# Optimization experiments

Hardware: AMD Instinct MI355X
Metric: run time of the kernel (lower is better)

Reference implementation:

```python
import jax, jax.numpy as jnp
import numpy as np

EMB_SIZE = 768
BLOCK_SIZE = 64
NUM_CLASS = 97
N = 4096
NUM_BLOCKS = EMB_SIZE // BLOCK_SIZE  # 12


def setup_inputs() -> dict:
    key = jax.random.key(0)
    k1, k2, k3 = jax.random.split(key, 3)
    head_embeddings = jax.random.normal(k1, (N, EMB_SIZE), dtype=jnp.float32)
    tail_embeddings = jax.random.normal(k2, (N, EMB_SIZE), dtype=jnp.float32)
    # xavier_uniform for [NUM_CLASS, EMB_SIZE*BLOCK_SIZE]
    fan_in = EMB_SIZE * BLOCK_SIZE
    fan_out = NUM_CLASS
    bound = float(np.sqrt(6.0 / (fan_in + fan_out)))
    W = jax.random.uniform(k3, (NUM_CLASS, EMB_SIZE * BLOCK_SIZE), dtype=jnp.float32,
                           minval=-bound, maxval=bound)
    b = jnp.full((NUM_CLASS,), 0.1, dtype=jnp.float32)
    return {"head_embeddings": head_embeddings, "tail_embeddings": tail_embeddings,
            "W": W, "b": b}


def reference(head_embeddings, tail_embeddings, W, b):
    n = head_embeddings.shape[0]
    b1 = head_embeddings.reshape(n, NUM_BLOCKS, BLOCK_SIZE)  # [N, K, S]
    b2 = tail_embeddings.reshape(n, NUM_BLOCKS, BLOCK_SIZE)  # [N, K, S]
    # block-wise outer product: [N, K, S, S] -> [N, K*S*S]
    bl = jnp.einsum('nki,nkj->nkij', b1, b2).reshape(n, EMB_SIZE * BLOCK_SIZE)
    logits = bl @ W.T + b  # [N, NUM_CLASS]
    return logits
```

## Files before the change

### kernel.cpp

```cpp
#include <hip/hip_runtime.h>
#include <hip/hip_bf16.h>
#include <stdint.h>

#define NROWS 4096
#define NCLS  97
#define EMB   768
#define KTOT  49152
#define OUT_ELEMS (NROWS * NCLS)
#define E_ELEMS  (NROWS * EMB)
#define NK32  (KTOT / 32)
#define WT_BYTES ((size_t)NK32 * 128 * 64)

typedef __attribute__((ext_vector_type(8)))  short short8;
typedef __attribute__((ext_vector_type(4)))  float floatx4;
typedef __bf16 bf16x2 __attribute__((ext_vector_type(2)));
typedef __bf16 bf16x8 __attribute__((ext_vector_type(8)));

__device__ __forceinline__ uint4 cvt8(float4 a, float4 b) {
  bf16x8 v;
  v[0] = (__bf16)a.x; v[1] = (__bf16)a.y; v[2] = (__bf16)a.z; v[3] = (__bf16)a.w;
  v[4] = (__bf16)b.x; v[5] = (__bf16)b.y; v[6] = (__bf16)b.z; v[7] = (__bf16)b.w;
  return __builtin_bit_cast(uint4, v);
}

__device__ __forceinline__ uint32_t mkbf2(float lo, float hi) {
  bf16x2 v; v[0] = (__bf16)lo; v[1] = (__bf16)hi;
  return __builtin_bit_cast(uint32_t, v);
}

__global__ void prep(const float* __restrict__ W, uint4* __restrict__ wt)
{
  const int nwt = NK32 * 128 * 4;
  int t = blockIdx.x * blockDim.x + threadIdx.x;
  if (t >= nwt) return;
  int eo = t & 3;
  int c  = (t >> 2) & 127;
  int kc = t >> 9;
  uint4 v = uint4{0u, 0u, 0u, 0u};
  if (c < NCLS) {
    const float4* p = (const float4*)(W + (size_t)c * KTOT + kc * 32 + eo * 8);
    v = cvt8(p[0], p[1]);
  }
  wt[t] = v;
}

__global__ __launch_bounds__(256, 2)
void bilinear_main(const float* __restrict__ b1f,
                   const float* __restrict__ b2f,
                   const char* __restrict__ Wt,
                   const float* __restrict__ biasg,
                   float* __restrict__ P,
                   float* __restrict__ outd,
                   int klen)
{
  const int tid  = threadIdx.x;
  const int w    = tid >> 6;
  const int l    = tid & 63;
  const int l15  = l & 15;
  const int quad = l >> 4;
  const int mhalf = w & 1;
  const int chalf = w >> 1;
  const bool cfull = (chalf == 0);
  const int bm = blockIdx.y;
  const int k0 = blockIdx.x * klen;

  int nrow[4];
#pragma unroll
  for (int rt = 0; rt < 4; ++rt) nrow[rt] = bm * 128 + mhalf * 64 + rt * 16 + l15;

  const char* wtl = Wt + (size_t)(k0 >> 5) * 8192
                       + (chalf * 64 + l15) * 64 + quad * 16;

  floatx4 acc[4][4];
#pragma unroll
  for (int rt = 0; rt < 4; ++rt)
#pragma unroll
    for (int ct = 0; ct < 4; ++ct)
      acc[rt][ct] = floatx4{0.f, 0.f, 0.f, 0.f};

  float b2r[4][2][8];
  int cur_k = -1;
  const int nwin = klen >> 6;

  for (int gwin = 0; gwin < nwin; gwin += 8) {
    const int kap0 = k0 + (gwin << 6);
    const int kblk = kap0 >> 12;
    const int i0   = (kap0 >> 6) & 63;
    if (kblk != cur_k) {
      cur_k = kblk;
#pragma unroll
      for (int rt = 0; rt < 4; ++rt)
#pragma unroll
        for (int kh = 0; kh < 2; ++kh) {
          const float* p = b2f + (size_t)nrow[rt] * EMB + kblk * 64 + kh * 32 + quad * 8;
          float4 v0 = ((const float4*)p)[0];
          float4 v1 = ((const float4*)p)[1];
          b2r[rt][kh][0] = v0.x; b2r[rt][kh][1] = v0.y;
          b2r[rt][kh][2] = v0.z; b2r[rt][kh][3] = v0.w;
          b2r[rt][kh][4] = v1.x; b2r[rt][kh][5] = v1.y;
          b2r[rt][kh][6] = v1.z; b2r[rt][kh][7] = v1.w;
        }
    }

#pragma unroll
    for (int ih = 0; ih < 2; ++ih) {
      float4 b1v[4];
#pragma unroll
      for (int rt = 0; rt < 4; ++rt)
        b1v[rt] = *(const float4*)(b1f + (size_t)nrow[rt] * EMB +
                                   kblk * 64 + i0 + ih * 4);

#pragma unroll
      for (int ii2 = 0; ii2 < 4; ++ii2) {
        const int iw = gwin + ih * 4 + ii2;
        const char* pw = wtl + (size_t)iw * 16384;

        float s[4];
#pragma unroll
        for (int rt = 0; rt < 4; ++rt)
          s[rt] = (&b1v[rt].x)[ii2];

#pragma unroll
        for (int kh = 0; kh < 2; ++kh) {
          short8 wf[4];
#pragma unroll
          for (int ct = 0; ct < 4; ++ct)
            if (ct < 3 || cfull)
              wf[ct] = __builtin_bit_cast(short8,
                         *(const uint4*)(pw + kh * 8192 + ct * 1024));
#pragma unroll
          for (int rt = 0; rt < 4; ++rt) {
            uint4 afr;
            afr.x = mkbf2(b2r[rt][kh][0] * s[rt], b2r[rt][kh][1] * s[rt]);
            afr.y = mkbf2(b2r[rt][kh][2] * s[rt], b2r[rt][kh][3] * s[rt]);
            afr.z = mkbf2(b2r[rt][kh][4] * s[rt], b2r[rt][kh][5] * s[rt]);
            afr.w = mkbf2(b2r[rt][kh][6] * s[rt], b2r[rt][kh][7] * s[rt]);
            short8 af = __builtin_bit_cast(short8, afr);
#pragma unroll
            for (int ct = 0; ct < 4; ++ct)
              if (ct < 3 || cfull)
                acc[rt][ct] = __builtin_amdgcn_mfma_f32_16x16x32_bf16(
                                  af, wf[ct], acc[rt][ct], 0, 0, 0);
          }
        }
      }
    }
  }

  if (P) {
    float* Pb = P + (size_t)blockIdx.x * OUT_ELEMS;
#pragma unroll
    for (int rt = 0; rt < 4; ++rt)
#pragma unroll
      for (int ct = 0; ct < 4; ++ct) {
        const int c = chalf * 64 + ct * 16 + l15;
        if (c < NCLS) {
#pragma unroll
          for (int r = 0; r < 4; ++r) {
            const int row = bm * 128 + mhalf * 64 + rt * 16 + quad * 4 + r;
            Pb[(size_t)row * NCLS + c] = acc[rt][ct][r];
          }
        }
      }
  } else {
#pragma unroll
    for (int rt = 0; rt < 4; ++rt)
#pragma unroll
      for (int ct = 0; ct < 4; ++ct) {
        const int c = chalf * 64 + ct * 16 + l15;
        if (c < NCLS) {
          const float bv = biasg[c];
#pragma unroll
          for (int r = 0; r < 4; ++r) {
            const int row = bm * 128 + mhalf * 64 + rt * 16 + quad * 4 + r;
            outd[(size_t)row * NCLS + c] = acc[rt][ct][r] + bv;
          }
        }
      }
  }
}

template<int KSC>
__global__ void reduce_bias_t(const float* __restrict__ P,
                              const float* __restrict__ biasg,
                              float* __restrict__ out)
{
  int i = blockIdx.x * blockDim.x + threadIdx.x;
  const int n4 = OUT_ELEMS / 4;
  if (i >= n4) return;
  int c0 = (i * 4) % NCLS;
  int c1 = c0 + 1 == NCLS ? 0 : c0 + 1;
  int c2 = c1 + 1 == NCLS ? 0 : c1 + 1;
  int c3 = c2 + 1 == NCLS ? 0 : c2 + 1;
  float4 s;
  s.x = biasg[c0]; s.y = biasg[c1]; s.z = biasg[c2]; s.w = biasg[c3];
  const float4* P4 = (const float4*)P;
#pragma unroll
  for (int t = 0; t < KSC; ++t) {
    float4 v = P4[(size_t)t * n4 + i];
    s.x += v.x; s.y += v.y; s.z += v.z; s.w += v.w;
  }
  ((float4*)out)[i] = s;
}

static void launch_reduce(int KS, const float* P, const float* bb, float* out,
                          hipStream_t stream) {
  const int nb = (OUT_ELEMS / 4 + 255) / 256;
  switch (KS) {
    case 16: reduce_bias_t<16><<<nb, 256, 0, stream>>>(P, bb, out); break;
    case 12: reduce_bias_t<12><<<nb, 256, 0, stream>>>(P, bb, out); break;
    case 8:  reduce_bias_t<8><<<nb, 256, 0, stream>>>(P, bb, out);  break;
    case 6:  reduce_bias_t<6><<<nb, 256, 0, stream>>>(P, bb, out);  break;
    case 4:  reduce_bias_t<4><<<nb, 256, 0, stream>>>(P, bb, out);  break;
    case 3:  reduce_bias_t<3><<<nb, 256, 0, stream>>>(P, bb, out);  break;
    case 2:  reduce_bias_t<2><<<nb, 256, 0, stream>>>(P, bb, out);  break;
    default: reduce_bias_t<1><<<nb, 256, 0, stream>>>(P, bb, out);  break;
  }
}

extern "C" void kernel_launch(void* const* d_in, const int* in_sizes, int n_in,
                              void* d_out, int out_size, void* d_ws, size_t ws_size,
                              hipStream_t stream) {
  const float* b1f = (const float*)d_in[0];
  const float* b2f = (const float*)d_in[1];
  const float* Wf  = (const float*)d_in[2];
  const float* bbf = (const float*)d_in[3];
  float* out = (float*)d_out;

  const size_t slice = (size_t)OUT_ELEMS * 4;
  static const int cands[] = {16, 12, 8, 6, 4, 3, 2, 1};
  const int NC = 8;

  int KS = 0;
  for (int i = 0; i < NC; ++i)
    if (WT_BYTES + (size_t)cands[i] * slice <= ws_size) { KS = cands[i]; break; }

  uint4* Wt = (uint4*)d_ws;
  const int nwt = NK32 * 128 * 4;

  prep<<<(nwt + 255) / 256, 256, 0, stream>>>(Wf, Wt);

  if (KS > 0) {
    float* P = (float*)((char*)d_ws + WT_BYTES);
    bilinear_main<<<dim3(KS, 32), 256, 0, stream>>>(
        b1f, b2f, (const char*)Wt, bbf, P, nullptr, KTOT / KS);
    launch_reduce(KS, P, bbf, out, stream);
  } else {
    bilinear_main<<<dim3(1, 32), 256, 0, stream>>>(
        b1f, b2f, (const char*)Wt, bbf, nullptr, out, KTOT);
  }
}
```

Measured before the change: 152.8 us.

## Switch to fp16 MFMA with packed fp16 A-build and double-buffered W fragment loads

Replaces the bf16 path with fp16: W is pre-converted to fp16, b2 is held as packed fp16 pairs, and the A fragment is built with packed half multiplies instead of fp32 multiplies plus bf16 conversion. This cuts the VALU work per MFMA. It also adds register double-buffering, loading the next window's W fragments before computing the current one so global-load latency overlaps MFMA work. The cost is more register pressure and fp16 range and precision risk: products are formed in fp16, where values can overflow or lose accuracy.

Result: no change. 151.9 us (-0.6%).

```diff
diff --git a/kernel.cpp b/kernel.cpp
--- a/kernel.cpp
+++ b/kernel.cpp
@@ -11,21 +11,15 @@
 #define NK32  (KTOT / 32)
 #define WT_BYTES ((size_t)NK32 * 128 * 64)
 
-typedef __attribute__((ext_vector_type(8)))  short short8;
 typedef __attribute__((ext_vector_type(4)))  float floatx4;
-typedef __bf16 bf16x2 __attribute__((ext_vector_type(2)));
-typedef __bf16 bf16x8 __attribute__((ext_vector_type(8)));
-
-__device__ __forceinline__ uint4 cvt8(float4 a, float4 b) {
-  bf16x8 v;
-  v[0] = (__bf16)a.x; v[1] = (__bf16)a.y; v[2] = (__bf16)a.z; v[3] = (__bf16)a.w;
-  v[4] = (__bf16)b.x; v[5] = (__bf16)b.y; v[6] = (__bf16)b.z; v[7] = (__bf16)b.w;
+typedef _Float16 f16x2 __attribute__((ext_vector_type(2)));
+typedef _Float16 f16x8 __attribute__((ext_vector_type(8)));
+
+__device__ __forceinline__ uint4 cvt8h(float4 a, float4 b) {
+  f16x8 v;
+  v[0] = (_Float16)a.x; v[1] = (_Float16)a.y; v[2] = (_Float16)a.z; v[3] = (_Float16)a.w;
+  v[4] = (_Float16)b.x; v[5] = (_Float16)b.y; v[6] = (_Float16)b.z; v[7] = (_Float16)b.w;
   return __builtin_bit_cast(uint4, v);
-}
-
-__device__ __forceinline__ uint32_t mkbf2(float lo, float hi) {
-  bf16x2 v; v[0] = (__bf16)lo; v[1] = (__bf16)hi;
-  return __builtin_bit_cast(uint32_t, v);
 }
 
 __global__ void prep(const float* __restrict__ W, uint4* __restrict__ wt)
@@ -39,7 +33,7 @@
   uint4 v = uint4{0u, 0u, 0u, 0u};
   if (c < NCLS) {
     const float4* p = (const float4*)(W + (size_t)c * KTOT + kc * 32 + eo * 8);
-    v = cvt8(p[0], p[1]);
+    v = cvt8h(p[0], p[1]);
   }
   wt[t] = v;
 }
@@ -78,9 +72,49 @@
     for (int ct = 0; ct < 4; ++ct)
       acc[rt][ct] = floatx4{0.f, 0.f, 0.f, 0.f};
 
-  float b2r[4][2][8];
+  f16x2 b2h[4][2][4];
+  f16x2 sv[4];
+  uint4 wfA[2][4], wfB[2][4];
+
+#define LOADWF(buf, iwv)  do {                                              \
+    const char* pw_ = wtl + (size_t)(iwv) * 16384;                          \
+    _Pragma("unroll")                                                       \
+    for (int kh_ = 0; kh_ < 2; ++kh_)                                       \
+      _Pragma("unroll")                                                     \
+      for (int ct_ = 0; ct_ < 4; ++ct_)                                     \
+        if (ct_ < 3 || cfull)                                               \
+          buf[kh_][ct_] = *(const uint4*)(pw_ + kh_ * 8192 + ct_ * 1024);   \
+  } while (0)
+
+#define COMPUTE(buf)  do {                                                  \
+    _Pragma("unroll")                                                       \
+    for (int kh_ = 0; kh_ < 2; ++kh_) {                                     \
+      _Pragma("unroll")                                                     \
+      for (int rt_ = 0; rt_ < 4; ++rt_) {                                   \
+        f16x2 p0 = sv[rt_] * b2h[rt_][kh_][0];                              \
+        f16x2 p1 = sv[rt_] * b2h[rt_][kh_][1];                              \
+        f16x2 p2 = sv[rt_] * b2h[rt_][kh_][2];                              \
+        f16x2 p3 = sv[rt_] * b2h[rt_][kh_][3];                              \
+        uint4 au;                                                           \
+        au.x = __builtin_bit_cast(uint32_t, p0);                            \
+        au.y = __builtin_bit_cast(uint32_t, p1);                            \
+        au.z = __builtin_bit_cast(uint32_t, p2);                            \
+        au.w = __builtin_bit_cast(uint32_t, p3);                            \
+        f16x8 af = __builtin_bit_cast(f16x8, au);                           \
+        _Pragma("unroll")                                                   \
+        for (int ct_ = 0; ct_ < 4; ++ct_)                                   \
+          if (ct_ < 3 || cfull)                                             \
+            acc[rt_][ct_] = __builtin_amdgcn_mfma_f32_16x16x32_f16(         \
+                af, __builtin_bit_cast(f16x8, buf[kh_][ct_]),               \
+                acc[rt_][ct_], 0, 0, 0);                                    \
+      }                                                                     \
+    }                                                                       \
+  } while (0)
+
   int cur_k = -1;
   const int nwin = klen >> 6;
+
+  LOADWF(wfA, 0);
 
   for (int gwin = 0; gwin < nwin; gwin += 8) {
     const int kap0 = k0 + (gwin << 6);
@@ -95,10 +129,10 @@
           const float* p = b2f + (size_t)nrow[rt] * EMB + kblk * 64 + kh * 32 + quad * 8;
           float4 v0 = ((const float4*)p)[0];
           float4 v1 = ((const float4*)p)[1];
-          b2r[rt][kh][0] = v0.x; b2r[rt][kh][1] = v0.y;
-          b2r[rt][kh][2] = v0.z; b2r[rt][kh][3] = v0.w;
-          b2r[rt][kh][4] = v1.x; b2r[rt][kh][5] = v1.y;
-          b2r[rt][kh][6] = v1.z; b2r[rt][kh][7] = v1.w;
+          b2h[rt][kh][0][0] = (_Float16)v0.x; b2h[rt][kh][0][1] = (_Float16)v0.y;
+          b2h[rt][kh][1][0] = (_Float16)v0.z; b2h[rt][kh][1][1] = (_Float16)v0.w;
+          b2h[rt][kh][2][0] = (_Float16)v1.x; b2h[rt][kh][2][1] = (_Float16)v1.y;
+          b2h[rt][kh][3][0] = (_Float16)v1.z; b2h[rt][kh][3][1] = (_Float16)v1.w;
         }
     }
 
@@ -112,40 +146,24 @@
 
 #pragma unroll
       for (int ii2 = 0; ii2 < 4; ++ii2) {
-        const int iw = gwin + ih * 4 + ii2;
-        const char* pw = wtl + (size_t)iw * 16384;
-
-        float s[4];
-#pragma unroll
-        for (int rt = 0; rt < 4; ++rt)
-          s[rt] = (&b1v[rt].x)[ii2];
-
-#pragma unroll
-        for (int kh = 0; kh < 2; ++kh) {
-          short8 wf[4];
-#pragma unroll
-          for (int ct = 0; ct < 4; ++ct)
-            if (ct < 3 || cfull)
-              wf[ct] = __builtin_bit_cast(short8,
-                         *(const uint4*)(pw + kh * 8192 + ct * 1024));
-#pragma unroll
-          for (int rt = 0; rt < 4; ++rt) {
-            uint4 afr;
-            afr.x = mkbf2(b2r[rt][kh][0] * s[rt], b2r[rt][kh][1] * s[rt]);
-            afr.y = mkbf2(b2r[rt][kh][2] * s[rt], b2r[rt][kh][3] * s[rt]);
-            afr.z = mkbf2(b2r[rt][kh][4] * s[rt], b2r[rt][kh][5] * s[rt]);
-            afr.w = mkbf2(b2r[rt][kh][6] * s[rt], b2r[rt][kh][7] * s[rt]);
-            short8 af = __builtin_bit_cast(short8, afr);
-#pragma unroll
-            for (int ct = 0; ct < 4; ++ct)
-              if (ct < 3 || cfull)
-                acc[rt][ct] = __builtin_amdgcn_mfma_f32_16x16x32_bf16(
-                                  af, wf[ct], acc[rt][ct], 0, 0, 0);
-          }
-        }
+        const int s  = ih * 4 + ii2;
+        const int iw = gwin + s;
+        int ipf = iw + 1;
+        if (ipf > nwin - 1) ipf = nwin - 1;
+
+#pragma unroll
+        for (int rt = 0; rt < 4; ++rt) {
+          _Float16 h = (_Float16)((&b1v[rt].x)[ii2]);
+          sv[rt][0] = h; sv[rt][1] = h;
+        }
+
+        if ((s & 1) == 0) { LOADWF(wfB, ipf); COMPUTE(wfA); }
+        else              { LOADWF(wfA, ipf); COMPUTE(wfB); }
       }
     }
   }
+#undef LOADWF
+#undef COMPUTE
 
   if (P) {
     float* Pb = P + (size_t)blockIdx.x * OUT_ELEMS;
```

## Stage W tiles through LDS with register prefetch and switch to fp16 packed math

Applied to the files above, without the earlier changes.

Each block now loads the per-window W tile cooperatively into shared memory, prefetching the next tile into registers while computing the current one. Previously each wave read W fragments straight from global memory. The A-operand outer product now uses packed fp16 multiplies instead of fp32 multiplies plus bf16 conversion, and the MFMA switches to the f16 variant. The change adds two block barriers per window and LDS traffic, and fp16 has a smaller dynamic range than bf16, which could affect accuracy.

Measured after the change: 214.2 us. 1.4x slower.

```diff
diff --git a/kernel.cpp b/kernel.cpp
--- a/kernel.cpp
+++ b/kernel.cpp
@@ -11,21 +11,15 @@
 #define NK32  (KTOT / 32)
 #define WT_BYTES ((size_t)NK32 * 128 * 64)
 
-typedef __attribute__((ext_vector_type(8)))  short short8;
 typedef __attribute__((ext_vector_type(4)))  float floatx4;
-typedef __bf16 bf16x2 __attribute__((ext_vector_type(2)));
-typedef __bf16 bf16x8 __attribute__((ext_vector_type(8)));
-
-__device__ __forceinline__ uint4 cvt8(float4 a, float4 b) {
-  bf16x8 v;
-  v[0] = (__bf16)a.x; v[1] = (__bf16)a.y; v[2] = (__bf16)a.z; v[3] = (__bf16)a.w;
-  v[4] = (__bf16)b.x; v[5] = (__bf16)b.y; v[6] = (__bf16)b.z; v[7] = (__bf16)b.w;
+typedef _Float16 f16x2 __attribute__((ext_vector_type(2)));
+typedef _Float16 f16x8 __attribute__((ext_vector_type(8)));
+
+__device__ __forceinline__ uint4 cvt8h(float4 a, float4 b) {
+  f16x8 v;
+  v[0] = (_Float16)a.x; v[1] = (_Float16)a.y; v[2] = (_Float16)a.z; v[3] = (_Float16)a.w;
+  v[4] = (_Float16)b.x; v[5] = (_Float16)b.y; v[6] = (_Float16)b.z; v[7] = (_Float16)b.w;
   return __builtin_bit_cast(uint4, v);
-}
-
-__device__ __forceinline__ uint32_t mkbf2(float lo, float hi) {
-  bf16x2 v; v[0] = (__bf16)lo; v[1] = (__bf16)hi;
-  return __builtin_bit_cast(uint32_t, v);
 }
 
 __global__ void prep(const float* __restrict__ W, uint4* __restrict__ wt)
@@ -39,7 +33,7 @@
   uint4 v = uint4{0u, 0u, 0u, 0u};
   if (c < NCLS) {
     const float4* p = (const float4*)(W + (size_t)c * KTOT + kc * 32 + eo * 8);
-    v = cvt8(p[0], p[1]);
+    v = cvt8h(p[0], p[1]);
   }
   wt[t] = v;
 }
@@ -64,12 +58,14 @@
   const int bm = blockIdx.y;
   const int k0 = blockIdx.x * klen;
 
+  __shared__ uint4 sW[1024];
+
   int nrow[4];
 #pragma unroll
   for (int rt = 0; rt < 4; ++rt) nrow[rt] = bm * 128 + mhalf * 64 + rt * 16 + l15;
 
-  const char* wtl = Wt + (size_t)(k0 >> 5) * 8192
-                       + (chalf * 64 + l15) * 64 + quad * 16;
+  const char* wtbase = Wt + (size_t)(k0 >> 5) * 8192;
+  const int rslot = chalf * 256 + l15 * 4 + quad;
 
   floatx4 acc[4][4];
 #pragma unroll
@@ -78,74 +74,117 @@
     for (int ct = 0; ct < 4; ++ct)
       acc[rt][ct] = floatx4{0.f, 0.f, 0.f, 0.f};
 
-  float b2r[4][2][8];
-  int cur_k = -1;
+  f16x2 b2h[4][2][4];
+  float4 b1cur[4], b1nxt[4];
+  uint4  wst[4];
+
+#define LOADB2(kbv) do {                                                      \
+    _Pragma("unroll")                                                         \
+    for (int rt_ = 0; rt_ < 4; ++rt_)                                         \
+      _Pragma("unroll")                                                       \
+      for (int kh_ = 0; kh_ < 2; ++kh_) {                                     \
+        const float* p_ = b2f + (size_t)nrow[rt_] * EMB + (kbv) * 64 +        \
+                          kh_ * 32 + quad * 8;                                \
+        float4 v0_ = ((const float4*)p_)[0];                                  \
+        float4 v1_ = ((const float4*)p_)[1];                                  \
+        b2h[rt_][kh_][0][0] = (_Float16)v0_.x; b2h[rt_][kh_][0][1] = (_Float16)v0_.y; \
+        b2h[rt_][kh_][1][0] = (_Float16)v0_.z; b2h[rt_][kh_][1][1] = (_Float16)v0_.w; \
+        b2h[rt_][kh_][2][0] = (_Float16)v1_.x; b2h[rt_][kh_][2][1] = (_Float16)v1_.y; \
+        b2h[rt_][kh_][3][0] = (_Float16)v1_.z; b2h[rt_][kh_][3][1] = (_Float16)v1_.w; \
+      }                                                                       \
+  } while (0)
+
   const int nwin = klen >> 6;
-
-  for (int gwin = 0; gwin < nwin; gwin += 8) {
-    const int kap0 = k0 + (gwin << 6);
-    const int kblk = kap0 >> 12;
-    const int i0   = (kap0 >> 6) & 63;
-    if (kblk != cur_k) {
-      cur_k = kblk;
+  const int ngrp = nwin >> 2;
+
+  {
+    const uint4* g0 = (const uint4*)wtbase;
+#pragma unroll
+    for (int it = 0; it < 4; ++it) wst[it] = g0[it * 256 + tid];
+#pragma unroll
+    for (int it = 0; it < 4; ++it) sW[it * 256 + tid] = wst[it];
+  }
+  int cur_kb = k0 >> 12;
+  LOADB2(cur_kb);
+#pragma unroll
+  for (int rt = 0; rt < 4; ++rt)
+    b1cur[rt] = *(const float4*)(b1f + (size_t)nrow[rt] * EMB +
+                                 cur_kb * 64 + ((k0 >> 6) & 63));
+  __syncthreads();
+
+  for (int gp = 0; gp < ngrp; ++gp) {
+    const int kap_g = k0 + gp * 256;
+    const int kb = kap_g >> 12;
+    if (kb != cur_kb) { cur_kb = kb; LOADB2(kb); }
+    {
+      const int h = (gp + 1 < ngrp) ? gp + 1 : gp;
+      const int kap_h = k0 + h * 256;
 #pragma unroll
       for (int rt = 0; rt < 4; ++rt)
-#pragma unroll
-        for (int kh = 0; kh < 2; ++kh) {
-          const float* p = b2f + (size_t)nrow[rt] * EMB + kblk * 64 + kh * 32 + quad * 8;
-          float4 v0 = ((const float4*)p)[0];
-          float4 v1 = ((const float4*)p)[1];
-          b2r[rt][kh][0] = v0.x; b2r[rt][kh][1] = v0.y;
-          b2r[rt][kh][2] = v0.z; b2r[rt][kh][3] = v0.w;
-          b2r[rt][kh][4] = v1.x; b2r[rt][kh][5] = v1.y;
-          b2r[rt][kh][6] = v1.z; b2r[rt][kh][7] = v1.w;
-        }
+        b1nxt[rt] = *(const float4*)(b1f + (size_t)nrow[rt] * EMB +
+                                     (kap_h >> 12) * 64 + ((kap_h >> 6) & 63));
     }
 
 #pragma unroll
-    for (int ih = 0; ih < 2; ++ih) {
-      float4 b1v[4];
-#pragma unroll
-      for (int rt = 0; rt < 4; ++rt)
-        b1v[rt] = *(const float4*)(b1f + (size_t)nrow[rt] * EMB +
-                                   kblk * 64 + i0 + ih * 4);
-
-#pragma unroll
-      for (int ii2 = 0; ii2 < 4; ++ii2) {
-        const int iw = gwin + ih * 4 + ii2;
-        const char* pw = wtl + (size_t)iw * 16384;
-
-        float s[4];
-#pragma unroll
-        for (int rt = 0; rt < 4; ++rt)
-          s[rt] = (&b1v[rt].x)[ii2];
-
-#pragma unroll
-        for (int kh = 0; kh < 2; ++kh) {
-          short8 wf[4];
+    for (int s = 0; s < 4; ++s) {
+      const int iw = gp * 4 + s;
+
+      if (iw + 1 < nwin) {
+        const uint4* gn = (const uint4*)(wtbase + (size_t)(iw + 1) * 16384);
+#pragma unroll
+        for (int it = 0; it < 4; ++it) wst[it] = gn[it * 256 + tid];
+      }
+
+      uint4 wf[2][4];
+#pragma unroll
+      for (int kh = 0; kh < 2; ++kh)
+#pragma unroll
+        for (int ct = 0; ct < 4; ++ct)
+          if (ct < 3 || cfull)
+            wf[kh][ct] = sW[kh * 512 + ct * 64 + rslot];
+
+      f16x2 sv[4];
+#pragma unroll
+      for (int rt = 0; rt < 4; ++rt) {
+        _Float16 h = (_Float16)((&b1cur[rt].x)[s]);
+        sv[rt][0] = h; sv[rt][1] = h;
+      }
+
+#pragma unroll
+      for (int kh = 0; kh < 2; ++kh)
+#pragma unroll
+        for (int rt = 0; rt < 4; ++rt) {
+          f16x2 p0 = sv[rt] * b2h[rt][kh][0];
+          f16x2 p1 = sv[rt] * b2h[rt][kh][1];
+          f16x2 p2 = sv[rt] * b2h[rt][kh][2];
+          f16x2 p3 = sv[rt] * b2h[rt][kh][3];
+          uint4 au;
+          au.x = __builtin_bit_cast(uint32_t, p0);
+          au.y = __builtin_bit_cast(uint32_t, p1);
+          au.z = __builtin_bit_cast(uint32_t, p2);
+          au.w = __builtin_bit_cast(uint32_t, p3);
+          f16x8 af = __builtin_bit_cast(f16x8, au);
 #pragma unroll
           for (int ct = 0; ct < 4; ++ct)
             if (ct < 3 || cfull)
-              wf[ct] = __builtin_bit_cast(short8,
-                         *(const uint4*)(pw + kh * 8192 + ct * 1024));
-#pragma unroll
-          for (int rt = 0; rt < 4; ++rt) {
-            uint4 afr;
-            afr.x = mkbf2(b2r[rt][kh][0] * s[rt], b2r[rt][kh][1] * s[rt]);
-            afr.y = mkbf2(b2r[rt][kh][2] * s[rt], b2r[rt][kh][3] * s[rt]);
-            afr.z = mkbf2(b2r[rt][kh][4] * s[rt], b2r[rt][kh][5] * s[rt]);
-            afr.w = mkbf2(b2r[rt][kh][6] * s[rt], b2r[rt][kh][7] * s[rt]);
-            short8 af = __builtin_bit_cast(short8, afr);
-#pragma unroll
-            for (int ct = 0; ct < 4; ++ct)
-              if (ct < 3 || cfull)
-                acc[rt][ct] = __builtin_amdgcn_mfma_f32_16x16x32_bf16(
-                                  af, wf[ct], acc[rt][ct], 0, 0, 0);
-          }
+              acc[rt][ct] = __builtin_amdgcn_mfma_f32_16x16x32_f16(
+                  af, __builtin_bit_cast(f16x8, wf[kh][ct]),
+                  acc[rt][ct], 0, 0, 0);
         }
-      }
+
+      __syncthreads();
+
+      if (iw + 1 < nwin) {
+#pragma unroll
+        for (int it = 0; it < 4; ++it) sW[it * 256 + tid] = wst[it];
+      }
+
+      __syncthreads();
     }
-  }
+#pragma unroll
+    for (int rt = 0; rt < 4; ++rt) b1cur[rt] = b1nxt[rt];
+  }
+#undef LOADB2
 
   if (P) {
     float* Pb = P + (size_t)blockIdx.x * OUT_ELEMS;
```
